# Kernel tuning notes

Hardware: AMD Instinct MI355X
Metric: run time of the kernel (lower is better)

The kernel has to match this reference:

```python
import jax, jax.numpy as jnp
import numpy as np

N, E, F, R, S = 20000, 320000, 64, 8, 10
AVG_NEIGH = 16.0


def setup_inputs() -> dict:
    key = jax.random.key(0)
    ks = jax.random.split(key, 16)
    inp = {
        "vectors": jax.random.normal(ks[0], (E, 3), jnp.float32),
        "node_feats": jax.random.normal(ks[1], (N, F, 4), jnp.float32),  # [N, F, 1(0e)+3(1o)]
        "node_specie": jax.random.randint(ks[2], (N,), 0, S),
        "radial_embedding": jax.random.normal(ks[3], (E, R), jnp.float32),
        "senders": jax.random.randint(ks[4], (E,), 0, N),
        "receivers": jax.random.randint(ks[5], (E,), 0, N),
        # residual FullyConnectedTensorProduct(feats, one-hot species 0e) == species-dep. linear per l
        "W_res_s": jax.random.normal(ks[6], (S, F, F), jnp.float32),
        "W_res_v": jax.random.normal(ks[7], (S, F, F), jnp.float32),
        # interaction block: input linear per l
        "W_in_s": jax.random.normal(ks[8], (F, F), jnp.float32),
        "W_in_v": jax.random.normal(ks[9], (F, F), jnp.float32),
        # radial MLP -> 5 CG tensor-product path weights per channel
        "mlp_w1": jax.random.normal(ks[10], (R, 64), jnp.float32),
        "mlp_w2": jax.random.normal(ks[11], (64, 5 * F), jnp.float32) / 8.0,
        # interaction block: output linear per l
        "W_out_s": jax.random.normal(ks[12], (F, F), jnp.float32),
        "W_out_v": jax.random.normal(ks[13], (F, F), jnp.float32),
        # symmetric product basis (correlation 3), species-dependent term weights
        "W_prod_s": jax.random.normal(ks[14], (S, 5, F), jnp.float32) * 0.3,
        "W_prod_v": jax.random.normal(ks[15], (S, 4, F), jnp.float32) * 0.3,
    }
    k2 = jax.random.split(jax.random.key(1), 3)
    inp["W_lin_s"] = jax.random.normal(k2[0], (F, F), jnp.float32)
    inp["W_lin_v"] = jax.random.normal(k2[1], (F, F), jnp.float32)
    inp["W_read"] = jax.random.normal(k2[2], (F, 1), jnp.float32)
    return inp


def _forward(vectors, node_feats, node_specie, radial_embedding, senders, receivers,
             W_res_s, W_res_v, W_in_s, W_in_v, mlp_w1, mlp_w2, W_out_s, W_out_v,
             W_prod_s, W_prod_v, W_lin_s, W_lin_v, W_read):
    inv_sf = 1.0 / jnp.sqrt(jnp.float32(F))
    s = node_feats[..., 0]          # [N,F]   0e channels
    v = node_feats[..., 1:]         # [N,F,3] 1o channels

    # --- residual connection: FCTP(feats, one-hot species 0e attrs) -> species-gated linear per l
    res_s = jnp.einsum('nf,ngf->ng', s, W_res_s[node_specie]) * inv_sf
    res_v = jnp.einsum('nfc,ngf->ngc', v, W_res_v[node_specie]) * inv_sf

    # --- InteractionBlock ---
    h_s = (s @ W_in_s) * inv_sf
    h_v = jnp.einsum('nfc,fg->ngc', v, W_in_v) * inv_sf

    # spherical harmonics up to max_ell=1: Y0 = 1, Y1 = unit edge vector
    r = jnp.sqrt(jnp.sum(vectors * vectors, -1) + 1e-12)
    Y1 = vectors / r[:, None]                                # [E,3]

    # radial MLP produces per-edge weights for the 5 CG paths:
    # (0e x Y0 -> 0e), (1o . Y1 -> 0e), (0e x Y1 -> 1o), (1o x Y0 -> 1o), (1o x Y1 -> 1o, cross)
    w = (jax.nn.silu(radial_embedding @ mlp_w1) @ mlp_w2).reshape(-1, 5, F)  # [E,5,F]

    ss = h_s[senders]                                        # [E,F]
    sv = h_v[senders]                                        # [E,F,3]
    dot = jnp.einsum('efc,ec->ef', sv, Y1)                   # [E,F]
    m_s = w[:, 0] * ss + w[:, 1] * dot                       # [E,F]
    m_v = (w[:, 2] * ss)[:, :, None] * Y1[:, None, :] \
        + w[:, 3][:, :, None] * sv \
        + w[:, 4][:, :, None] * jnp.cross(sv, Y1[:, None, :])  # [E,F,3]

    agg_s = jnp.zeros_like(h_s).at[receivers].add(m_s) / AVG_NEIGH
    agg_v = jnp.zeros_like(h_v).at[receivers].add(m_v) / AVG_NEIGH
    a_s = (agg_s @ W_out_s) * inv_sf
    a_v = jnp.einsum('nfc,fg->ngc', agg_v, W_out_v) * inv_sf

    # --- EquivariantProductBasisBlock: correlation-3 symmetric contraction, species-dependent ---
    vv = jnp.sum(a_v * a_v, -1)                              # [N,F] invariant |v|^2
    Wp = W_prod_s[node_specie]                               # [N,5,F]
    p_s = (Wp[:, 0] * a_s + Wp[:, 1] * a_s ** 2 + Wp[:, 2] * a_s ** 3
           + Wp[:, 3] * vv + Wp[:, 4] * a_s * vv)
    Wv = W_prod_v[node_specie]                               # [N,4,F]
    p_v = (Wv[:, 0] + Wv[:, 1] * a_s + Wv[:, 2] * a_s ** 2 + Wv[:, 3] * vv)[:, :, None] * a_v

    f_s = (p_s @ W_lin_s) * inv_sf + res_s
    f_v = jnp.einsum('nfc,fg->ngc', p_v, W_lin_v) * inv_sf + res_v

    # --- LinearReadoutBlock (output_irreps = 0e), 1 head ---
    node_out = ((f_s @ W_read) * inv_sf)[:, None, :]         # [N, heads=1, 1]
    new_feats = jnp.concatenate([f_s[..., None], f_v], axis=-1)  # [N,F,4]
    return node_out, new_feats


def reference(vectors, node_feats, node_specie, radial_embedding, senders, receivers,
              W_res_s, W_res_v, W_in_s, W_in_v, mlp_w1, mlp_w2, W_out_s, W_out_v,
              W_prod_s, W_prod_v, W_lin_s, W_lin_v, W_read):
    return _forward(vectors, node_feats, node_specie, radial_embedding, senders, receivers,
                    W_res_s, W_res_v, W_in_s, W_in_v, mlp_w1, mlp_w2, W_out_s, W_out_v,
                    W_prod_s, W_prod_v, W_lin_s, W_lin_v, W_read)
```

## Files before the change

### kernel.cpp

```cpp
#include <hip/hip_runtime.h>
#include <math.h>

#define NN 20000
#define NE 320000
#define NF (NN*64)
#define TB 16

typedef float v2f __attribute__((ext_vector_type(2)));

#if __has_builtin(__builtin_elementwise_fma)
#define PKFMA(a,b,c) __builtin_elementwise_fma(a,b,c)
#else
static __device__ __forceinline__ v2f PKFMA(v2f a, v2f b, v2f c){
  v2f r; r.x = fmaf(a.x,b.x,c.x); r.y = fmaf(a.y,b.y,c.y); return r;
}
#endif

__global__ __launch_bounds__(256) void k_hist_prep(
    const int* __restrict__ receivers, int* __restrict__ count, int* __restrict__ rank,
    const float* __restrict__ Ws, const float* __restrict__ Wv,
    float* __restrict__ Wst, float* __restrict__ Wvt)
{
  int e = blockIdx.x*256 + threadIdx.x;
  rank[e] = atomicAdd(&count[receivers[e]], 1);
  if(blockIdx.x < 160){
    int i = blockIdx.x*256 + threadIdx.x;
    int spec = i >> 12;
    int g = (i >> 6) & 63;
    int f = i & 63;
    Wst[spec*4096 + f*64 + g] = Ws[i];
    Wvt[spec*4096 + f*64 + g] = Wv[i];
  }
}

__global__ __launch_bounds__(1024) void k_scan(const int* __restrict__ count,
                                               int* __restrict__ offset)
{
  __shared__ int part[1024];
  int t = threadIdx.x;
  const int PER = 20;
  int base = t*PER;
  int loc[PER];
  int s = 0;
  #pragma unroll
  for(int i=0;i<PER;++i){
    int idx = base+i;
    int v = (idx < NN) ? count[idx] : 0;
    loc[i] = v; s += v;
  }
  part[t] = s;
  __syncthreads();
  for(int off=1; off<1024; off<<=1){
    int v = (t>=off) ? part[t-off] : 0;
    __syncthreads();
    part[t] += v;
    __syncthreads();
  }
  int run = t ? part[t-1] : 0;
  #pragma unroll
  for(int i=0;i<PER;++i){
    int idx = base+i;
    if(idx < NN) offset[idx] = run;
    run += loc[i];
  }
  if(t==1023) offset[NN] = part[1023];
}

__global__ __launch_bounds__(256) void k_scatter(
    const int* __restrict__ senders, const int* __restrict__ receivers,
    const float* __restrict__ vectors, const float* __restrict__ radial,
    const int* __restrict__ offset, const int* __restrict__ rank,
    float* __restrict__ rec)
{
  int e = blockIdx.x*256 + threadIdx.x;
  int r = receivers[e];
  int slot = offset[r] + rank[e];
  float vx = vectors[e*3], vy = vectors[e*3+1], vz = vectors[e*3+2];
  float rinv = rsqrtf(vx*vx + vy*vy + vz*vz + 1e-12f);
  float4 ra = *(const float4*)(radial + (size_t)e*8);
  float4 rb = *(const float4*)(radial + (size_t)e*8 + 4);
  float* rp = rec + (size_t)slot*16;
  float4 w0; w0.x = vx*rinv; w0.y = vy*rinv; w0.z = vz*rinv; w0.w = __int_as_float(senders[e]);
  float4 w3; w3.x = __int_as_float(r); w3.y = 0.f; w3.z = 0.f; w3.w = 0.f;
  *(float4*)(rp)      = w0;
  *(float4*)(rp + 4)  = ra;
  *(float4*)(rp + 8)  = rb;
  *(float4*)(rp + 12) = w3;
}

__global__ __launch_bounds__(256) void k_node_pre(
    const float* __restrict__ node_feats, const float* __restrict__ W_in_s,
    const float* __restrict__ W_in_v, float* __restrict__ h)
{
  __shared__ float sh[16][4][64];
  int wave = threadIdx.x >> 6, lane = threadIdx.x & 63;
  int nb = blockIdx.x*16 + wave*4;
  #pragma unroll
  for(int k=0;k<4;++k){
    int nd = wave*4 + k;
    float4 nf = *(const float4*)(node_feats + (size_t)((nb+k)*64 + lane)*4);
    sh[nd][0][lane]=nf.x; sh[nd][1][lane]=nf.y; sh[nd][2][lane]=nf.z; sh[nd][3][lane]=nf.w;
  }
  __syncthreads();
  float as[4]={0,0,0,0}, a0[4]={0,0,0,0}, a1[4]={0,0,0,0}, a2[4]={0,0,0,0};
  for(int f=0; f<64; ++f){
    float ws = W_in_s[f*64+lane], wv = W_in_v[f*64+lane];
    #pragma unroll
    for(int k=0;k<4;++k){
      int nd = wave*4 + k;
      as[k] = fmaf(sh[nd][0][f], ws, as[k]);
      a0[k] = fmaf(sh[nd][1][f], wv, a0[k]);
      a1[k] = fmaf(sh[nd][2][f], wv, a1[k]);
      a2[k] = fmaf(sh[nd][3][f], wv, a2[k]);
    }
  }
  #pragma unroll
  for(int k=0;k<4;++k){
    float4 o4; o4.x = as[k]*0.125f; o4.y = a0[k]*0.125f;
    o4.z = a1[k]*0.125f; o4.w = a2[k]*0.125f;
    *(float4*)(h + (size_t)((nb+k)*64 + lane)*4) = o4;
  }
}

__global__ __launch_bounds__(256, 1) void k_edge(
    const float* __restrict__ rec,
    const float* __restrict__ mlp_w1, const float* __restrict__ mlp_w2,
    const float* __restrict__ h, float* __restrict__ agg)
{
  __shared__ float recS[4][256];
  __shared__ float hid[4][64][18];
  int tid = threadIdx.x;
  int wave = tid >> 6, lane = tid & 63;
  int e0 = (blockIdx.x*4 + wave)*TB;

  *(float4*)&recS[wave][lane*4] = *(const float4*)(rec + (size_t)e0*16 + lane*4);

  float4 hv4[8];
  #pragma unroll
  for(int p=0;p<8;++p){
    int snd = __float_as_int(recS[wave][p*16+3]);
    hv4[p] = *(const float4*)(h + (size_t)(snd*64 + lane)*4);
  }

  float wl[8];
  #pragma unroll
  for(int r=0;r<8;++r) wl[r] = mlp_w1[r*64+lane];

  #pragma unroll
  for(int t=0;t<TB;++t){
    float acc = 0.f;
    #pragma unroll
    for(int r=0;r<8;++r) acc = fmaf(recS[wave][t*16+4+r], wl[r], acc);
    hid[wave][lane][t] = acc / (1.f + __expf(-acc));
  }

  v2f wv[5][8];
  #pragma unroll
  for(int j=0;j<5;++j)
    #pragma unroll
    for(int tp=0;tp<8;++tp) wv[j][tp] = (v2f){0.f, 0.f};

  for(int hh=0; hh<64; hh+=2){
    float b0[5], b1[5];
    #pragma unroll
    for(int j=0;j<5;++j){
      b0[j] = mlp_w2[hh*320     + j*64 + lane];
      b1[j] = mlp_w2[(hh+1)*320 + j*64 + lane];
    }
    #pragma unroll
    for(int tp=0;tp<8;++tp){
      v2f h0 = *(const v2f*)&hid[wave][hh][2*tp];
      v2f h1 = *(const v2f*)&hid[wave][hh+1][2*tp];
      #pragma unroll
      for(int j=0;j<5;++j){
        v2f bb0 = {b0[j], b0[j]};
        v2f bb1 = {b1[j], b1[j]};
        wv[j][tp] = PKFMA(bb0, h0, wv[j][tp]);
        wv[j][tp] = PKFMA(bb1, h1, wv[j][tp]);
      }
    }
  }

  float as_=0.f, av0=0.f, av1=0.f, av2=0.f;
  int cur = __float_as_int(recS[wave][12]);
  #pragma unroll
  for(int t=0;t<TB;++t){
    float4 hc = hv4[t&7];
    if(t < 8){
      int snd = __float_as_int(recS[wave][(t+8)*16+3]);
      hv4[t&7] = *(const float4*)(h + (size_t)(snd*64 + lane)*4);
    }
    int rcv = __float_as_int(recS[wave][t*16+12]);
    if(rcv != cur){
      size_t ro = (size_t)cur*256 + lane;
      atomicAdd(&agg[ro],     as_);
      atomicAdd(&agg[ro+64],  av0);
      atomicAdd(&agg[ro+128], av1);
      atomicAdd(&agg[ro+192], av2);
      as_=0.f; av0=0.f; av1=0.f; av2=0.f;
      cur = rcv;
    }
    float y0=recS[wave][t*16], y1=recS[wave][t*16+1], y2=recS[wave][t*16+2];
    float ss=hc.x, sv0=hc.y, sv1=hc.z, sv2=hc.w;
    float dot = sv0*y0 + sv1*y1 + sv2*y2;
    float wt0 = wv[0][t>>1][t&1], wt1 = wv[1][t>>1][t&1];
    float wt2 = wv[2][t>>1][t&1], wt3 = wv[3][t>>1][t&1], wt4 = wv[4][t>>1][t&1];
    as_ += wt0*ss + wt1*dot;
    float w2s = wt2*ss;
    av0 += w2s*y0 + wt3*sv0 + wt4*(sv1*y2 - sv2*y1);
    av1 += w2s*y1 + wt3*sv1 + wt4*(sv2*y0 - sv0*y2);
    av2 += w2s*y2 + wt3*sv2 + wt4*(sv0*y1 - sv1*y0);
  }
  size_t ro = (size_t)cur*256 + lane;
  atomicAdd(&agg[ro],     as_);
  atomicAdd(&agg[ro+64],  av0);
  atomicAdd(&agg[ro+128], av1);
  atomicAdd(&agg[ro+192], av2);
}

__global__ __launch_bounds__(256) void k_node_post(
  const float* __restrict__ node_feats, const int* __restrict__ specie,
  const float* __restrict__ agg,
  const float* __restrict__ Wrst, const float* __restrict__ Wrvt,
  const float* __restrict__ W_out_s, const float* __restrict__ W_out_v,
  const float* __restrict__ W_prod_s, const float* __restrict__ W_prod_v,
  const float* __restrict__ W_lin_s, const float* __restrict__ W_lin_v,
  const float* __restrict__ W_read, float* __restrict__ out_node,
  float* __restrict__ out_feats)
{
  __shared__ float shA[16][4][64];
  __shared__ float shS[16][4][64];
  int wave = threadIdx.x >> 6, lane = threadIdx.x & 63;
  int nb = blockIdx.x*16 + wave*4;
  #pragma unroll
  for(int k=0;k<4;++k){
    int nd = wave*4 + k;
    size_t o = (size_t)(nb+k)*256 + lane;
    shA[nd][0][lane] = agg[o]      * (1.f/16.f);
    shA[nd][1][lane] = agg[o+64]   * (1.f/16.f);
    shA[nd][2][lane] = agg[o+128]  * (1.f/16.f);
    shA[nd][3][lane] = agg[o+192]  * (1.f/16.f);
    float4 nf = *(const float4*)(node_feats + (size_t)((nb+k)*64 + lane)*4);
    shS[nd][0][lane]=nf.x; shS[nd][1][lane]=nf.y; shS[nd][2][lane]=nf.z; shS[nd][3][lane]=nf.w;
  }
  int spec[4];
  #pragma unroll
  for(int k=0;k<4;++k) spec[k] = specie[nb+k];
  __syncthreads();
  float a_s[4]={0,0,0,0}, a0[4]={0,0,0,0}, a1[4]={0,0,0,0}, a2[4]={0,0,0,0};
  float r_s[4]={0,0,0,0}, r0[4]={0,0,0,0}, r1[4]={0,0,0,0}, r2[4]={0,0,0,0};
  for(int f=0; f<64; ++f){
    float wos = W_out_s[f*64+lane], wov = W_out_v[f*64+lane];
    #pragma unroll
    for(int k=0;k<4;++k){
      int nd = wave*4 + k;
      a_s[k] = fmaf(shA[nd][0][f], wos, a_s[k]);
      a0[k]  = fmaf(shA[nd][1][f], wov, a0[k]);
      a1[k]  = fmaf(shA[nd][2][f], wov, a1[k]);
      a2[k]  = fmaf(shA[nd][3][f], wov, a2[k]);
    }
    #pragma unroll
    for(int k=0;k<4;++k){
      int nd = wave*4 + k;
      float wrs = Wrst[spec[k]*4096 + f*64 + lane];
      float wrv = Wrvt[spec[k]*4096 + f*64 + lane];
      r_s[k] = fmaf(shS[nd][0][f], wrs, r_s[k]);
      r0[k]  = fmaf(shS[nd][1][f], wrv, r0[k]);
      r1[k]  = fmaf(shS[nd][2][f], wrv, r1[k]);
      r2[k]  = fmaf(shS[nd][3][f], wrv, r2[k]);
    }
  }
  __syncthreads();
  #pragma unroll
  for(int k=0;k<4;++k){
    int nd = wave*4 + k;
    float A_s = a_s[k]*0.125f, A0 = a0[k]*0.125f, A1 = a1[k]*0.125f, A2 = a2[k]*0.125f;
    float vv = A0*A0 + A1*A1 + A2*A2;
    float as2 = A_s*A_s;
    const float* Wp = W_prod_s + spec[k]*320;
    float p_s = Wp[lane]*A_s + Wp[64+lane]*as2 + Wp[128+lane]*as2*A_s
              + Wp[192+lane]*vv + Wp[256+lane]*A_s*vv;
    const float* Wq = W_prod_v + spec[k]*256;
    float coef = Wq[lane] + Wq[64+lane]*A_s + Wq[128+lane]*as2 + Wq[192+lane]*vv;
    shS[nd][0][lane] = p_s;
    shS[nd][1][lane] = coef*A0;
    shS[nd][2][lane] = coef*A1;
    shS[nd][3][lane] = coef*A2;
  }
  __syncthreads();
  float lfs[4]={0,0,0,0}, lf0[4]={0,0,0,0}, lf1[4]={0,0,0,0}, lf2[4]={0,0,0,0};
  for(int f=0; f<64; ++f){
    float wls = W_lin_s[f*64+lane], wlv = W_lin_v[f*64+lane];
    #pragma unroll
    for(int k=0;k<4;++k){
      int nd = wave*4 + k;
      lfs[k] = fmaf(shS[nd][0][f], wls, lfs[k]);
      lf0[k] = fmaf(shS[nd][1][f], wlv, lf0[k]);
      lf1[k] = fmaf(shS[nd][2][f], wlv, lf1[k]);
      lf2[k] = fmaf(shS[nd][3][f], wlv, lf2[k]);
    }
  }
  float wr = W_read[lane];
  #pragma unroll
  for(int k=0;k<4;++k){
    int n = nb + k;
    float FS = lfs[k]*0.125f + r_s[k]*0.125f;
    float F0 = lf0[k]*0.125f + r0[k]*0.125f;
    float F1 = lf1[k]*0.125f + r1[k]*0.125f;
    float F2 = lf2[k]*0.125f + r2[k]*0.125f;
    float x = FS * wr;
    #pragma unroll
    for(int off=32; off; off>>=1) x += __shfl_down(x, off);
    if(lane==0) out_node[n] = x*0.125f;
    float4 o4; o4.x=FS; o4.y=F0; o4.z=F1; o4.w=F2;
    *(float4*)(out_feats + (size_t)(n*64+lane)*4) = o4;
  }
}

extern "C" void kernel_launch(void* const* d_in, const int* in_sizes, int n_in,
                              void* d_out, int out_size, void* d_ws, size_t ws_size,
                              hipStream_t stream) {
  const float* vectors    = (const float*)d_in[0];
  const float* node_feats = (const float*)d_in[1];
  const int*   node_specie= (const int*)  d_in[2];
  const float* radial     = (const float*)d_in[3];
  const int*   senders    = (const int*)  d_in[4];
  const int*   receivers  = (const int*)  d_in[5];
  const float* W_res_s    = (const float*)d_in[6];
  const float* W_res_v    = (const float*)d_in[7];
  const float* W_in_s     = (const float*)d_in[8];
  const float* W_in_v     = (const float*)d_in[9];
  const float* mlp_w1     = (const float*)d_in[10];
  const float* mlp_w2     = (const float*)d_in[11];
  const float* W_out_s    = (const float*)d_in[12];
  const float* W_out_v    = (const float*)d_in[13];
  const float* W_prod_s   = (const float*)d_in[14];
  const float* W_prod_v   = (const float*)d_in[15];
  const float* W_lin_s    = (const float*)d_in[16];
  const float* W_lin_v    = (const float*)d_in[17];
  const float* W_read     = (const float*)d_in[18];

  float* ws   = (float*)d_ws;
  float* h    = ws;
  float* agg  = ws + 4*(size_t)NF;
  float* Wrst = ws + 8*(size_t)NF;
  float* Wrvt = Wrst + 40960;
  float* rec  = Wrvt + 40960;
  int*   rank   = (int*)(rec + 16*(size_t)NE);
  int*   offset = rank + NE;
  int*   count  = offset + NN + 1;

  hipMemsetAsync(agg,   0, (size_t)4*NF*sizeof(float), stream);
  hipMemsetAsync(count, 0, (size_t)NN*sizeof(int), stream);
  k_hist_prep<<<NE/256, 256, 0, stream>>>(receivers, count, rank,
                                          W_res_s, W_res_v, Wrst, Wrvt);
  k_scan     <<<1,     1024, 0, stream>>>(count, offset);
  k_scatter  <<<NE/256, 256, 0, stream>>>(senders, receivers, vectors, radial,
                                          offset, rank, rec);
  k_node_pre<<<NN/16, 256, 0, stream>>>(node_feats, W_in_s, W_in_v, h);
  k_edge<<<NE/64, 256, 0, stream>>>(rec, mlp_w1, mlp_w2, h, agg);
  k_node_post<<<NN/16, 256, 0, stream>>>(node_feats, node_specie, agg,
                                         Wrst, Wrvt, W_out_s, W_out_v,
                                         W_prod_s, W_prod_v, W_lin_s, W_lin_v,
                                         W_read, (float*)d_out, (float*)d_out + NN);
}
```

Baseline: 469.0 us.

## Fuse node pre-linear into histogram kernel and split edge MLP into halves

Merges the node input-linear kernel with the receiver histogram and weight-transpose kernel into one launch, using block index ranges to pick the role. The edge kernel now computes the radial MLP weights and gathers sender features eight edges at a time instead of sixteen, and drops the launch_bounds minimum of one block. This is meant to cut register pressure and raise occupancy, and to save one kernel launch. The cost is that mlp_w2 is re-read for each half, and the latency hiding from the earlier prefetch of the second gather batch is lost.

Result: no change. 465.1 us (-0.8%).

```diff
diff --git a/kernel.cpp b/kernel.cpp
--- a/kernel.cpp
+++ b/kernel.cpp
@@ -16,20 +16,54 @@
 }
 #endif
 
-__global__ __launch_bounds__(256) void k_hist_prep(
+__global__ __launch_bounds__(256) void k_pre(
+    const float* __restrict__ node_feats, const float* __restrict__ W_in_s,
+    const float* __restrict__ W_in_v, float* __restrict__ h,
     const int* __restrict__ receivers, int* __restrict__ count, int* __restrict__ rank,
     const float* __restrict__ Ws, const float* __restrict__ Wv,
     float* __restrict__ Wst, float* __restrict__ Wvt)
 {
-  int e = blockIdx.x*256 + threadIdx.x;
-  rank[e] = atomicAdd(&count[receivers[e]], 1);
-  if(blockIdx.x < 160){
-    int i = blockIdx.x*256 + threadIdx.x;
-    int spec = i >> 12;
-    int g = (i >> 6) & 63;
-    int f = i & 63;
-    Wst[spec*4096 + f*64 + g] = Ws[i];
-    Wvt[spec*4096 + f*64 + g] = Wv[i];
+  __shared__ float sh[16][4][64];
+  if(blockIdx.x >= 1250){
+    int b = blockIdx.x - 1250;
+    int e = b*256 + threadIdx.x;
+    rank[e] = atomicAdd(&count[receivers[e]], 1);
+    if(b < 160){
+      int i = b*256 + threadIdx.x;
+      int spec = i >> 12;
+      int g = (i >> 6) & 63;
+      int f = i & 63;
+      Wst[spec*4096 + f*64 + g] = Ws[i];
+      Wvt[spec*4096 + f*64 + g] = Wv[i];
+    }
+    return;
+  }
+  int wave = threadIdx.x >> 6, lane = threadIdx.x & 63;
+  int nb = blockIdx.x*16 + wave*4;
+  #pragma unroll
+  for(int k=0;k<4;++k){
+    int nd = wave*4 + k;
+    float4 nf = *(const float4*)(node_feats + (size_t)((nb+k)*64 + lane)*4);
+    sh[nd][0][lane]=nf.x; sh[nd][1][lane]=nf.y; sh[nd][2][lane]=nf.z; sh[nd][3][lane]=nf.w;
+  }
+  __syncthreads();
+  float as[4]={0,0,0,0}, a0[4]={0,0,0,0}, a1[4]={0,0,0,0}, a2[4]={0,0,0,0};
+  for(int f=0; f<64; ++f){
+    float ws = W_in_s[f*64+lane], wv = W_in_v[f*64+lane];
+    #pragma unroll
+    for(int k=0;k<4;++k){
+      int nd = wave*4 + k;
+      as[k] = fmaf(sh[nd][0][f], ws, as[k]);
+      a0[k] = fmaf(sh[nd][1][f], wv, a0[k]);
+      a1[k] = fmaf(sh[nd][2][f], wv, a1[k]);
+      a2[k] = fmaf(sh[nd][3][f], wv, a2[k]);
+    }
+  }
+  #pragma unroll
+  for(int k=0;k<4;++k){
+    float4 o4; o4.x = as[k]*0.125f; o4.y = a0[k]*0.125f;
+    o4.z = a1[k]*0.125f; o4.w = a2[k]*0.125f;
+    *(float4*)(h + (size_t)((nb+k)*64 + lane)*4) = o4;
   }
 }
 
@@ -88,41 +122,7 @@
   *(float4*)(rp + 12) = w3;
 }
 
-__global__ __launch_bounds__(256) void k_node_pre(
-    const float* __restrict__ node_feats, const float* __restrict__ W_in_s,
-    const float* __restrict__ W_in_v, float* __restrict__ h)
-{
-  __shared__ float sh[16][4][64];
-  int wave = threadIdx.x >> 6, lane = threadIdx.x & 63;
-  int nb = blockIdx.x*16 + wave*4;
-  #pragma unroll
-  for(int k=0;k<4;++k){
-    int nd = wave*4 + k;
-    float4 nf = *(const float4*)(node_feats + (size_t)((nb+k)*64 + lane)*4);
-    sh[nd][0][lane]=nf.x; sh[nd][1][lane]=nf.y; sh[nd][2][lane]=nf.z; sh[nd][3][lane]=nf.w;
-  }
-  __syncthreads();
-  float as[4]={0,0,0,0}, a0[4]={0,0,0,0}, a1[4]={0,0,0,0}, a2[4]={0,0,0,0};
-  for(int f=0; f<64; ++f){
-    float ws = W_in_s[f*64+lane], wv = W_in_v[f*64+lane];
-    #pragma unroll
-    for(int k=0;k<4;++k){
-      int nd = wave*4 + k;
-      as[k] = fmaf(sh[nd][0][f], ws, as[k]);
-      a0[k] = fmaf(sh[nd][1][f], wv, a0[k]);
-      a1[k] = fmaf(sh[nd][2][f], wv, a1[k]);
-      a2[k] = fmaf(sh[nd][3][f], wv, a2[k]);
-    }
-  }
-  #pragma unroll
-  for(int k=0;k<4;++k){
-    float4 o4; o4.x = as[k]*0.125f; o4.y = a0[k]*0.125f;
-    o4.z = a1[k]*0.125f; o4.w = a2[k]*0.125f;
-    *(float4*)(h + (size_t)((nb+k)*64 + lane)*4) = o4;
-  }
-}
-
-__global__ __launch_bounds__(256, 1) void k_edge(
+__global__ __launch_bounds__(256) void k_edge(
     const float* __restrict__ rec,
     const float* __restrict__ mlp_w1, const float* __restrict__ mlp_w2,
     const float* __restrict__ h, float* __restrict__ agg)
@@ -135,13 +135,6 @@
 
   *(float4*)&recS[wave][lane*4] = *(const float4*)(rec + (size_t)e0*16 + lane*4);
 
-  float4 hv4[8];
-  #pragma unroll
-  for(int p=0;p<8;++p){
-    int snd = __float_as_int(recS[wave][p*16+3]);
-    hv4[p] = *(const float4*)(h + (size_t)(snd*64 + lane)*4);
-  }
-
   float wl[8];
   #pragma unroll
   for(int r=0;r<8;++r) wl[r] = mlp_w1[r*64+lane];
@@ -154,62 +147,72 @@
     hid[wave][lane][t] = acc / (1.f + __expf(-acc));
   }
 
-  v2f wv[5][8];
-  #pragma unroll
-  for(int j=0;j<5;++j)
-    #pragma unroll
-    for(int tp=0;tp<8;++tp) wv[j][tp] = (v2f){0.f, 0.f};
-
-  for(int hh=0; hh<64; hh+=2){
-    float b0[5], b1[5];
-    #pragma unroll
-    for(int j=0;j<5;++j){
-      b0[j] = mlp_w2[hh*320     + j*64 + lane];
-      b1[j] = mlp_w2[(hh+1)*320 + j*64 + lane];
-    }
-    #pragma unroll
-    for(int tp=0;tp<8;++tp){
-      v2f h0 = *(const v2f*)&hid[wave][hh][2*tp];
-      v2f h1 = *(const v2f*)&hid[wave][hh+1][2*tp];
+  float as_=0.f, av0=0.f, av1=0.f, av2=0.f;
+  int cur = __float_as_int(recS[wave][12]);
+
+  #pragma unroll 1
+  for(int half=0; half<2; ++half){
+    int tb = half*8;
+
+    float4 hv4[8];
+    #pragma unroll
+    for(int p=0;p<8;++p){
+      int snd = __float_as_int(recS[wave][(tb+p)*16+3]);
+      hv4[p] = *(const float4*)(h + (size_t)(snd*64 + lane)*4);
+    }
+
+    v2f wv[5][4];
+    #pragma unroll
+    for(int j=0;j<5;++j)
+      #pragma unroll
+      for(int tp=0;tp<4;++tp) wv[j][tp] = (v2f){0.f, 0.f};
+
+    for(int hh=0; hh<64; hh+=2){
+      float b0[5], b1[5];
       #pragma unroll
       for(int j=0;j<5;++j){
-        v2f bb0 = {b0[j], b0[j]};
-        v2f bb1 = {b1[j], b1[j]};
-        wv[j][tp] = PKFMA(bb0, h0, wv[j][tp]);
-        wv[j][tp] = PKFMA(bb1, h1, wv[j][tp]);
+        b0[j] = mlp_w2[hh*320     + j*64 + lane];
+        b1[j] = mlp_w2[(hh+1)*320 + j*64 + lane];
       }
-    }
-  }
-
-  float as_=0.f, av0=0.f, av1=0.f, av2=0.f;
-  int cur = __float_as_int(recS[wave][12]);
-  #pragma unroll
-  for(int t=0;t<TB;++t){
-    float4 hc = hv4[t&7];
-    if(t < 8){
-      int snd = __float_as_int(recS[wave][(t+8)*16+3]);
-      hv4[t&7] = *(const float4*)(h + (size_t)(snd*64 + lane)*4);
-    }
-    int rcv = __float_as_int(recS[wave][t*16+12]);
-    if(rcv != cur){
-      size_t ro = (size_t)cur*256 + lane;
-      atomicAdd(&agg[ro],     as_);
-      atomicAdd(&agg[ro+64],  av0);
-      atomicAdd(&agg[ro+128], av1);
-      atomicAdd(&agg[ro+192], av2);
-      as_=0.f; av0=0.f; av1=0.f; av2=0.f;
-      cur = rcv;
-    }
-    float y0=recS[wave][t*16], y1=recS[wave][t*16+1], y2=recS[wave][t*16+2];
-    float ss=hc.x, sv0=hc.y, sv1=hc.z, sv2=hc.w;
-    float dot = sv0*y0 + sv1*y1 + sv2*y2;
-    float wt0 = wv[0][t>>1][t&1], wt1 = wv[1][t>>1][t&1];
-    float wt2 = wv[2][t>>1][t&1], wt3 = wv[3][t>>1][t&1], wt4 = wv[4][t>>1][t&1];
-    as_ += wt0*ss + wt1*dot;
-    float w2s = wt2*ss;
-    av0 += w2s*y0 + wt3*sv0 + wt4*(sv1*y2 - sv2*y1);
-    av1 += w2s*y1 + wt3*sv1 + wt4*(sv2*y0 - sv0*y2);
-    av2 += w2s*y2 + wt3*sv2 + wt4*(sv0*y1 - sv1*y0);
+      #pragma unroll
+      for(int tp=0;tp<4;++tp){
+        v2f h0 = *(const v2f*)&hid[wave][hh][tb + 2*tp];
+        v2f h1 = *(const v2f*)&hid[wave][hh+1][tb + 2*tp];
+        #pragma unroll
+        for(int j=0;j<5;++j){
+          v2f bb0 = {b0[j], b0[j]};
+          v2f bb1 = {b1[j], b1[j]};
+          wv[j][tp] = PKFMA(bb0, h0, wv[j][tp]);
+          wv[j][tp] = PKFMA(bb1, h1, wv[j][tp]);
+        }
+      }
+    }
+
+    #pragma unroll
+    for(int i=0;i<8;++i){
+      int t = tb + i;
+      float4 hc = hv4[i];
+      int rcv = __float_as_int(recS[wave][t*16+12]);
+      if(rcv != cur){
+        size_t ro = (size_t)cur*256 + lane;
+        atomicAdd(&agg[ro],     as_);
+        atomicAdd(&agg[ro+64],  av0);
+        atomicAdd(&agg[ro+128], av1);
+        atomicAdd(&agg[ro+192], av2);
+        as_=0.f; av0=0.f; av1=0.f; av2=0.f;
+        cur = rcv;
+      }
+      float y0=recS[wave][t*16], y1=recS[wave][t*16+1], y2=recS[wave][t*16+2];
+      float ss=hc.x, sv0=hc.y, sv1=hc.z, sv2=hc.w;
+      float dot = sv0*y0 + sv1*y1 + sv2*y2;
+      float wt0 = wv[0][i>>1][i&1], wt1 = wv[1][i>>1][i&1];
+      float wt2 = wv[2][i>>1][i&1], wt3 = wv[3][i>>1][i&1], wt4 = wv[4][i>>1][i&1];
+      as_ += wt0*ss + wt1*dot;
+      float w2s = wt2*ss;
+      av0 += w2s*y0 + wt3*sv0 + wt4*(sv1*y2 - sv2*y1);
+      av1 += w2s*y1 + wt3*sv1 + wt4*(sv2*y0 - sv0*y2);
+      av2 += w2s*y2 + wt3*sv2 + wt4*(sv0*y1 - sv1*y0);
+    }
   }
   size_t ro = (size_t)cur*256 + lane;
   atomicAdd(&agg[ro],     as_);
@@ -352,12 +355,12 @@
 
   hipMemsetAsync(agg,   0, (size_t)4*NF*sizeof(float), stream);
   hipMemsetAsync(count, 0, (size_t)NN*sizeof(int), stream);
-  k_hist_prep<<<NE/256, 256, 0, stream>>>(receivers, count, rank,
-                                          W_res_s, W_res_v, Wrst, Wrvt);
-  k_scan     <<<1,     1024, 0, stream>>>(count, offset);
-  k_scatter  <<<NE/256, 256, 0, stream>>>(senders, receivers, vectors, radial,
-                                          offset, rank, rec);
-  k_node_pre<<<NN/16, 256, 0, stream>>>(node_feats, W_in_s, W_in_v, h);
+  k_pre<<<2500, 256, 0, stream>>>(node_feats, W_in_s, W_in_v, h,
+                                  receivers, count, rank,
+                                  W_res_s, W_res_v, Wrst, Wrvt);
+  k_scan   <<<1,     1024, 0, stream>>>(count, offset);
+  k_scatter<<<NE/256, 256, 0, stream>>>(senders, receivers, vectors, radial,
+                                        offset, rank, rec);
   k_edge<<<NE/64, 256, 0, stream>>>(rec, mlp_w1, mlp_w2, h, agg);
   k_node_post<<<NN/16, 256, 0, stream>>>(node_feats, node_specie, agg,
                                          Wrst, Wrvt, W_out_s, W_out_v,
```
